# Performance work log

Measured on AMD Instinct MI355X. Metric: run time of the kernel, lower is better.

The kernel has to match this reference:

```python
import jax, jax.numpy as jnp
import numpy as np

IMG_H, IMG_W = 432.0, 768.0
B, N = 8, 1_000_000


def setup_inputs() -> dict:
    key = jax.random.key(0)
    k1, k2 = jax.random.split(key)
    scores = jax.random.uniform(k1, (B, N, 1), dtype=jnp.float32)
    # center-format boxes (x, y, w, h) roughly in image coords so masks fire
    scale = jnp.array([IMG_W, IMG_H, 256.0, 256.0], dtype=jnp.float32)
    rps = jax.random.uniform(k2, (B, N, 4), dtype=jnp.float32) * scale
    return {"scores": scores, "rps": rps, "n_train_pre_nms": 12000}


def _anchors_clip(boxes):
    # boxes: [B, N, 4] in (cx, cy, w, h)
    cx, cy, w, h = boxes[..., 0], boxes[..., 1], boxes[..., 2], boxes[..., 3]
    x1 = jnp.clip(cx - w * 0.5, 0.0, IMG_W)
    x2 = jnp.clip(cx + w * 0.5, 0.0, IMG_W)
    y1 = jnp.clip(cy - h * 0.5, 0.0, IMG_H)
    y2 = jnp.clip(cy + h * 0.5, 0.0, IMG_H)
    nw = x2 - x1
    nh = y2 - y1
    nx = x1 + nw * 0.5
    ny = y1 + nh * 0.5
    return jnp.stack([nx, ny, nw, nh], axis=-1)


def reference(scores, rps, n_train_pre_nms):
    rois = _anchors_clip(rps)                                   # [B, N, 4]
    mask = ((rois[..., 2] > 16.0) & (rois[..., 3] > 16.0))
    s = scores * mask.astype(scores.dtype)[..., None]           # [B, N, 1]
    # full descending argsort along anchor dim, keep top n_train_pre_nms
    order = jnp.argsort(-s[..., 0], axis=1)[:, :n_train_pre_nms]  # [B, K]
    rois_sel = jnp.take_along_axis(rois, order[..., None], axis=1)  # [B, K, 4]
    s_sel = jnp.take_along_axis(s, order[..., None], axis=1)        # [B, K, 1]
    return rois_sel, s_sel
```

## Files before the change

kernel.cpp:

```cpp
#include <hip/hip_runtime.h>
#include <stdint.h>

#define BATCH    8
#define NITEMS   1000000
#define NTHR     125000
#define NBLKS    489
#define NC       64
#define NF       4096
#define NF8      8192
#define SBASE    62
#define THRESH   0.96875f
#define MID63    0.984375f
#define BUFCAP   512
#define CANDCAP  65536
#define CANDCAP2 262144
#define CAPC     131072
#define IMG_W    768.0f
#define IMG_H    432.0f

typedef unsigned long long ull;

static __device__ __forceinline__ float clip0(float v, float hi) {
    return fminf(fmaxf(v, 0.0f), hi);
}
static __device__ __forceinline__ int cbin(float s) {
    int g = (int)(s * (float)NC);
    return g > NC - 1 ? NC - 1 : (g < 0 ? 0 : g);
}
static __device__ __forceinline__ int fbin(float s, int g) {
    int f = (int)(s * (float)(NC * NF)) - g * NF;
    return f > NF - 1 ? NF - 1 : (f < 0 ? 0 : f);
}
static __device__ __forceinline__ unsigned mkbits(float4 box, float s) {
    float x1 = clip0(box.x - box.z * 0.5f, IMG_W);
    float x2 = clip0(box.x + box.z * 0.5f, IMG_W);
    float y1 = clip0(box.y - box.w * 0.5f, IMG_H);
    float y2 = clip0(box.y + box.w * 0.5f, IMG_H);
    bool m = ((x2 - x1) > 16.0f) && ((y2 - y1) > 16.0f);
    return __float_as_uint(m ? s : 0.0f);
}
static __device__ __forceinline__ int g8of(float s) {
    int cb = (s >= MID63) ? 63 : 62;
    return (cb - SBASE) * NF + fbin(s, cb);
}

__global__ __launch_bounds__(256)
void k_scores(const float* __restrict__ scores,
              const float4* __restrict__ rps,
              ull* __restrict__ clist,
              unsigned* __restrict__ fhist8g,
              unsigned* __restrict__ rawCnt,
              unsigned* __restrict__ ovf) {
    __shared__ ull buf[BUFCAP];
    __shared__ unsigned blkCnt, gBase;
    const int b = blockIdx.y, tid = threadIdx.x;
    const int t = blockIdx.x * 256 + tid;
    const int lane = tid & 63;
    if (tid == 0) blkCnt = 0u;
    __syncthreads();
    const float4* sp4 = (const float4*)(scores + (size_t)b * NITEMS);
    float4 a0 = make_float4(0, 0, 0, 0), a1 = make_float4(0, 0, 0, 0);
    const bool act = (t < NTHR);
    if (act) { a0 = sp4[2 * t]; a1 = sp4[2 * t + 1]; }
    float sv[8] = {a0.x, a0.y, a0.z, a0.w, a1.x, a1.y, a1.z, a1.w};
    const int i0 = t * 8;
    #pragma unroll
    for (int j = 0; j < 8; ++j) {
        bool q = act && (sv[j] >= THRESH);
        ull m = __ballot(q);
        if (m) {
            unsigned pre = (unsigned)__popcll(m & ((1ULL << lane) - 1ULL));
            int leader = __ffsll((long long)m) - 1;
            unsigned bse = 0;
            if (lane == leader) bse = atomicAdd(&blkCnt, (unsigned)__popcll(m));
            bse = (unsigned)__shfl((int)bse, leader);
            if (q) {
                unsigned s2 = bse + pre;
                if (s2 < BUFCAP)
                    buf[s2] = ((ull)__float_as_uint(sv[j]) << 32) |
                              (unsigned)(~(unsigned)(i0 + j));
            }
        }
    }
    __syncthreads();
    unsigned n = blkCnt;
    if (n > BUFCAP) { if (tid == 0) atomicOr(&ovf[b], 1u); n = BUFCAP; }
    if (tid == 0) gBase = atomicAdd(&rawCnt[b], n);
    __syncthreads();
    const unsigned gb = gBase;
    for (unsigned i = tid; i < n; i += 256) {
        unsigned slot = gb + i;
        if (slot >= CANDCAP) break;
        ull key = buf[i];
        unsigned idx = ~((unsigned)key);
        float4 box = rps[(size_t)b * NITEMS + idx];
        float s = __uint_as_float((unsigned)(key >> 32));
        if (mkbits(box, s)) {
            atomicAdd(&fhist8g[b * NF8 + g8of(s)], 1u);
            clist[(size_t)b * CANDCAP + slot] = key;
        } else {
            clist[(size_t)b * CANDCAP + slot] = 0ull;
        }
    }
}

__global__ __launch_bounds__(1024)
void k_mid(const float* __restrict__ scores,
           const float4* __restrict__ rps,
           const ull* __restrict__ clist,
           ull* __restrict__ clist2,
           const unsigned* __restrict__ rawCnt,
           const unsigned* __restrict__ ovf,
           const unsigned* __restrict__ fhist8g,
           unsigned* __restrict__ fsuf8g,
           unsigned* __restrict__ csuf64g,
           unsigned* __restrict__ chist64g,
           unsigned* __restrict__ fsufFg,
           unsigned* __restrict__ fhistFg,
           unsigned* __restrict__ meta,
           ull* __restrict__ cand,
           int K) {
    const int b = blockIdx.x, tid = threadIdx.x;
    __shared__ unsigned h[NF8];
    __shared__ unsigned sc[1024];
    __shared__ unsigned smallA[NC], smallB[NC];
    __shared__ unsigned s_fb8, s_tot, s_cbb, s_nab, s_n2;

    unsigned cw[8], pin[8], run = 0;
    const unsigned* hb = fhist8g + b * NF8;
    #pragma unroll
    for (int k = 0; k < 8; ++k) {
        cw[k] = hb[NF8 - 1 - (tid * 8 + k)];
        run += cw[k]; pin[k] = run;
    }
    sc[tid] = run; __syncthreads();
    unsigned x = run;
    for (int off = 1; off < 1024; off <<= 1) {
        unsigned tv = (tid >= off) ? sc[tid - off] : 0u;
        __syncthreads();
        x += tv; sc[tid] = x;
        __syncthreads();
    }
    const unsigned exclBase = x - run;
    const unsigned alive = sc[1023];
    if (tid == 0) { s_fb8 = 0u; s_tot = alive; }
    __syncthreads();
    #pragma unroll
    for (int k = 0; k < 8; ++k) {
        int g = NF8 - 1 - (tid * 8 + k);
        unsigned excl = exclBase + pin[k] - cw[k];
        fsuf8g[b * NF8 + g] = excl;
        h[g] = excl;
        if (excl < (unsigned)K && excl + cw[k] >= (unsigned)K) {
            s_fb8 = (unsigned)g; s_tot = excl + cw[k];
        }
    }
    __syncthreads();
    const unsigned rawN0 = rawCnt[b];
    unsigned N = rawN0 > CANDCAP ? CANDCAP : rawN0;
    const bool fast = (alive >= (unsigned)K) && (ovf[b] == 0u) &&
                      (rawN0 <= (unsigned)CANDCAP) && (s_tot <= (unsigned)CAPC);
    if (tid == 0) {
        meta[b * 8 + 4] = fast ? 1u : 0u;
        meta[b * 8 + 2] = s_fb8;
        meta[b * 8 + 3] = s_tot;
    }
    __syncthreads();
    if (fast) {
        const unsigned fb8v = s_fb8;
        const size_t c0 = (size_t)b * CANDCAP;
        for (unsigned i = tid; i < N; i += 1024) {
            ull key = clist[c0 + i];
            if (!key) continue;
            float s = __uint_as_float((unsigned)(key >> 32));
            int g8 = g8of(s);
            if ((unsigned)g8 < fb8v) continue;
            unsigned slot = atomicAdd(&h[g8], 1u);
            if (slot < CAPC) cand[(size_t)b * CAPC + slot] = key;
        }
        return;
    }
    if (tid < NC) smallA[tid] = 0u;
    __syncthreads();
    const size_t base = (size_t)b * NITEMS;
    for (int i = tid; i < NITEMS; i += 1024) {
        unsigned bits = mkbits(rps[base + i], scores[base + i]);
        if (bits) atomicAdd(&smallA[cbin(__uint_as_float(bits))], 1u);
    }
    __syncthreads();
    if (tid == 0) {
        unsigned runc = 0, cbb = 0, nab = 0; bool found = false;
        for (int g = NC - 1; g >= 0; --g) {
            unsigned c = smallA[g];
            csuf64g[b * NC + g] = runc; chist64g[b * NC + g] = c;
            smallB[g] = runc;
            if (!found && runc < (unsigned)K && runc + c >= (unsigned)K) {
                cbb = (unsigned)g; nab = runc; found = true;
            }
            runc += c;
        }
        s_cbb = cbb; s_nab = nab; s_n2 = 0u;
        meta[b * 8 + 0] = cbb; meta[b * 8 + 1] = nab;
    }
    __syncthreads();
    const unsigned cbb = s_cbb, nab = s_nab;
    if (tid < NC) smallA[tid] = smallB[tid];
    for (int k = tid; k < NF; k += 1024) h[k] = 0u;
    __syncthreads();
    for (int i = tid; i < NITEMS; i += 1024) {
        unsigned bits = mkbits(rps[base + i], scores[base + i]);
        if (!bits) continue;
        float s = __uint_as_float(bits);
        int g = cbin(s);
        if ((unsigned)g < cbb) continue;
        ull key = ((ull)bits << 32) | (unsigned)(~(unsigned)i);
        if ((unsigned)g > cbb) {
            unsigned slot = atomicAdd(&smallA[g], 1u);
            if (slot < CAPC) cand[(size_t)b * CAPC + slot] = key;
        } else {
            unsigned s2 = atomicAdd(&s_n2, 1u);
            if (s2 < CANDCAP2) clist2[(size_t)b * CANDCAP2 + s2] = key;
            atomicAdd(&h[fbin(s, (int)cbb)], 1u);
        }
    }
    __syncthreads();
    unsigned n2 = s_n2 > CANDCAP2 ? CANDCAP2 : s_n2;
    unsigned fcw[4], fpin[4], frun = 0;
    #pragma unroll
    for (int k = 0; k < 4; ++k) {
        fcw[k] = h[NF - 1 - (tid * 4 + k)];
        frun += fcw[k]; fpin[k] = frun;
    }
    sc[tid] = frun; __syncthreads();
    unsigned fx = frun;
    for (int off = 1; off < 1024; off <<= 1) {
        unsigned tv = (tid >= off) ? sc[tid - off] : 0u;
        __syncthreads();
        fx += tv; sc[tid] = fx;
        __syncthreads();
    }
    const unsigned fexcl = fx - frun;
    const unsigned ftot = sc[1023];
    if (tid == 0) { s_fb8 = 0u; s_tot = nab + ftot; }
    __syncthreads();
    #pragma unroll
    for (int k = 0; k < 4; ++k) {
        int g = NF - 1 - (tid * 4 + k);
        unsigned excl = fexcl + fpin[k] - fcw[k];
        fsufFg[b * NF + g] = excl; fhistFg[b * NF + g] = fcw[k];
        unsigned t0 = nab + excl;
        if (t0 < (unsigned)K && t0 + fcw[k] >= (unsigned)K) {
            s_fb8 = (unsigned)g; s_tot = t0 + fcw[k];
        }
        h[g] = nab + excl;
    }
    __syncthreads();
    if (tid == 0) { meta[b * 8 + 2] = s_fb8; meta[b * 8 + 3] = s_tot; }
    __syncthreads();
    const unsigned fbv = s_fb8;
    for (unsigned i = tid; i < n2; i += 1024) {
        ull key = clist2[(size_t)b * CANDCAP2 + i];
        unsigned bits = (unsigned)(key >> 32);
        float s = __uint_as_float(bits);
        int f = fbin(s, (int)cbb);
        if ((unsigned)f < fbv) continue;
        unsigned slot = atomicAdd(&h[f], 1u);
        if (slot < CAPC) cand[(size_t)b * CAPC + slot] = key;
    }
}

__global__ __launch_bounds__(256)
void k_rank_out(const ull* __restrict__ cand,
                const unsigned* __restrict__ meta,
                const unsigned* __restrict__ fsuf8g,
                const unsigned* __restrict__ fhist8g,
                const unsigned* __restrict__ csuf64g,
                const unsigned* __restrict__ chist64g,
                const unsigned* __restrict__ fsufFg,
                const unsigned* __restrict__ fhistFg,
                const float4* __restrict__ rps,
                float* __restrict__ out,
                int K) {
    const int b = blockIdx.y;
    unsigned total = meta[b * 8 + 3];
    if (total > CAPC) total = CAPC;
    const unsigned fast = meta[b * 8 + 4];
    for (unsigned p = blockIdx.x * 256 + threadIdx.x; p < total;
         p += gridDim.x * 256) {
        const ull key = cand[(size_t)b * CAPC + p];
        const float s = __uint_as_float((unsigned)(key >> 32));
        unsigned sbase, scnt;
        if (fast) {
            int g8 = g8of(s);
            sbase = fsuf8g[b * NF8 + g8];
            scnt  = fhist8g[b * NF8 + g8];
        } else {
            const unsigned cbb = meta[b * 8 + 0], nab = meta[b * 8 + 1];
            int g = cbin(s);
            if ((unsigned)g > cbb) {
                sbase = csuf64g[b * NC + g];
                scnt  = chist64g[b * NC + g];
            } else {
                int f = fbin(s, (int)g);
                sbase = nab + fsufFg[b * NF + f];
                scnt  = fhistFg[b * NF + f];
            }
        }
        unsigned send = sbase + scnt;
        if (send > total) send = total;
        unsigned rank = sbase;
        for (unsigned j = sbase; j < send; ++j)
            rank += (cand[(size_t)b * CAPC + j] > key) ? 1u : 0u;
        if (rank < (unsigned)K) {
            unsigned idx = ~((unsigned)key);
            if (idx >= (unsigned)NITEMS) idx = 0;
            float4 box = rps[(size_t)b * NITEMS + idx];
            float x1 = clip0(box.x - box.z * 0.5f, IMG_W);
            float x2 = clip0(box.x + box.z * 0.5f, IMG_W);
            float y1 = clip0(box.y - box.w * 0.5f, IMG_H);
            float y2 = clip0(box.y + box.w * 0.5f, IMG_H);
            float nw = x2 - x1, nh = y2 - y1;
            float nx = x1 + nw * 0.5f, ny = y1 + nh * 0.5f;
            ((float4*)out)[(size_t)b * K + rank] = make_float4(nx, ny, nw, nh);
            out[(size_t)BATCH * K * 4 + (size_t)b * K + rank] = s;
        }
    }
}

extern "C" void kernel_launch(void* const* d_in, const int* in_sizes, int n_in,
                              void* d_out, int out_size, void* d_ws, size_t ws_size,
                              hipStream_t stream) {
    const float*  scores = (const float*)d_in[0];
    const float4* rps    = (const float4*)d_in[1];
    const int K = out_size / (BATCH * 5);

    uint8_t* w = (uint8_t*)d_ws;
    ull* clist        = (ull*)(w);
    ull* cand         = (ull*)(w +  4500000);
    ull* clist2       = (ull*)(w + 13000000);
    unsigned* fhist8g = (unsigned*)(w + 30000000);
    unsigned* rawCnt  = (unsigned*)(w + 30262144);
    unsigned* ovf     = (unsigned*)(w + 30262176);
    unsigned* fsuf8g  = (unsigned*)(w + 30400000);
    unsigned* meta    = (unsigned*)(w + 30700000);
    unsigned* csuf64g = (unsigned*)(w + 30701000);
    unsigned* chist64g= (unsigned*)(w + 30704000);
    unsigned* fsufFg  = (unsigned*)(w + 30710000);
    unsigned* fhistFg = (unsigned*)(w + 30850000);

    hipMemsetAsync(fhist8g, 0, 262208, stream);
    k_scores<<<dim3(NBLKS, BATCH), dim3(256), 0, stream>>>(scores, rps, clist,
                                                           fhist8g, rawCnt, ovf);
    k_mid<<<dim3(BATCH), dim3(1024), 0, stream>>>(scores, rps, clist, clist2,
                                                  rawCnt, ovf, fhist8g, fsuf8g,
                                                  csuf64g, chist64g, fsufFg, fhistFg,
                                                  meta, cand, K);
    k_rank_out<<<dim3(128, BATCH), dim3(256), 0, stream>>>(cand, meta, fsuf8g, fhist8g,
                                                           csuf64g, chist64g, fsufFg,
                                                           fhistFg, rps,
                                                           (float*)d_out, K);
}
```

Baseline: 91.74 us.

## Build fine histogram in k_mid shared memory instead of global atomics

Moves the fine-bin histogram construction from global atomics in k_scores into a shared-memory histogram pass inside k_mid, which rereads the candidate list. The 256KB memset is replaced by a tiny zeroing kernel that only clears the counters, and k_mid writes the histogram out for later kernels. This removes global atomic contention and a large memset, at the cost of an extra candidate-list scan in the single-block-per-batch k_mid.

```diff
diff --git a/kernel.cpp b/kernel.cpp
--- a/kernel.cpp
+++ b/kernel.cpp
@@ -44,11 +44,15 @@
     return (cb - SBASE) * NF + fbin(s, cb);
 }
 
+__global__ __launch_bounds__(64)
+void k_zero(unsigned* __restrict__ rawCnt, unsigned* __restrict__ ovf) {
+    if (threadIdx.x < BATCH) { rawCnt[threadIdx.x] = 0u; ovf[threadIdx.x] = 0u; }
+}
+
 __global__ __launch_bounds__(256)
 void k_scores(const float* __restrict__ scores,
               const float4* __restrict__ rps,
               ull* __restrict__ clist,
-              unsigned* __restrict__ fhist8g,
               unsigned* __restrict__ rawCnt,
               unsigned* __restrict__ ovf) {
     __shared__ ull buf[BUFCAP];
@@ -95,12 +99,7 @@
         unsigned idx = ~((unsigned)key);
         float4 box = rps[(size_t)b * NITEMS + idx];
         float s = __uint_as_float((unsigned)(key >> 32));
-        if (mkbits(box, s)) {
-            atomicAdd(&fhist8g[b * NF8 + g8of(s)], 1u);
-            clist[(size_t)b * CANDCAP + slot] = key;
-        } else {
-            clist[(size_t)b * CANDCAP + slot] = 0ull;
-        }
+        clist[(size_t)b * CANDCAP + slot] = mkbits(box, s) ? key : 0ull;
     }
 }
 
@@ -111,7 +110,7 @@
            ull* __restrict__ clist2,
            const unsigned* __restrict__ rawCnt,
            const unsigned* __restrict__ ovf,
-           const unsigned* __restrict__ fhist8g,
+           unsigned* __restrict__ fhist8g,
            unsigned* __restrict__ fsuf8g,
            unsigned* __restrict__ csuf64g,
            unsigned* __restrict__ chist64g,
@@ -126,11 +125,22 @@
     __shared__ unsigned smallA[NC], smallB[NC];
     __shared__ unsigned s_fb8, s_tot, s_cbb, s_nab, s_n2;
 
+    for (int k = tid; k < NF8; k += 1024) h[k] = 0u;
+    __syncthreads();
+    const unsigned rawN0 = rawCnt[b];
+    unsigned N = rawN0 > CANDCAP ? CANDCAP : rawN0;
+    const size_t c0 = (size_t)b * CANDCAP;
+    for (unsigned i = tid; i < N; i += 1024) {
+        ull key = clist[c0 + i];
+        if (!key) continue;
+        float s = __uint_as_float((unsigned)(key >> 32));
+        atomicAdd(&h[g8of(s)], 1u);
+    }
+    __syncthreads();
     unsigned cw[8], pin[8], run = 0;
-    const unsigned* hb = fhist8g + b * NF8;
     #pragma unroll
     for (int k = 0; k < 8; ++k) {
-        cw[k] = hb[NF8 - 1 - (tid * 8 + k)];
+        cw[k] = h[NF8 - 1 - (tid * 8 + k)];
         run += cw[k]; pin[k] = run;
     }
     sc[tid] = run; __syncthreads();
@@ -150,14 +160,18 @@
         int g = NF8 - 1 - (tid * 8 + k);
         unsigned excl = exclBase + pin[k] - cw[k];
         fsuf8g[b * NF8 + g] = excl;
-        h[g] = excl;
+        fhist8g[b * NF8 + g] = cw[k];
         if (excl < (unsigned)K && excl + cw[k] >= (unsigned)K) {
             s_fb8 = (unsigned)g; s_tot = excl + cw[k];
         }
     }
     __syncthreads();
-    const unsigned rawN0 = rawCnt[b];
-    unsigned N = rawN0 > CANDCAP ? CANDCAP : rawN0;
+    #pragma unroll
+    for (int k = 0; k < 8; ++k) {
+        int g = NF8 - 1 - (tid * 8 + k);
+        h[g] = exclBase + pin[k] - cw[k];
+    }
+    __syncthreads();
     const bool fast = (alive >= (unsigned)K) && (ovf[b] == 0u) &&
                       (rawN0 <= (unsigned)CANDCAP) && (s_tot <= (unsigned)CAPC);
     if (tid == 0) {
@@ -168,7 +182,6 @@
     __syncthreads();
     if (fast) {
         const unsigned fb8v = s_fb8;
-        const size_t c0 = (size_t)b * CANDCAP;
         for (unsigned i = tid; i < N; i += 1024) {
             ull key = clist[c0 + i];
             if (!key) continue;
@@ -348,9 +361,9 @@
     unsigned* fsufFg  = (unsigned*)(w + 30710000);
     unsigned* fhistFg = (unsigned*)(w + 30850000);
 
-    hipMemsetAsync(fhist8g, 0, 262208, stream);
+    k_zero<<<dim3(1), dim3(64), 0, stream>>>(rawCnt, ovf);
     k_scores<<<dim3(NBLKS, BATCH), dim3(256), 0, stream>>>(scores, rps, clist,
-                                                           fhist8g, rawCnt, ovf);
+                                                           rawCnt, ovf);
     k_mid<<<dim3(BATCH), dim3(1024), 0, stream>>>(scores, rps, clist, clist2,
                                                   rawCnt, ovf, fhist8g, fsuf8g,
                                                   csuf64g, chist64g, fsufFg, fhistFg,
```

Measured after the change: 98.32 us. 7.2% more time.

## Fuse mid and rank kernels, drop global atomics and memset via per-block slots

Applied to the files above, without the earlier changes.

Each score block now writes its candidates into a fixed per-block slot region and records its count, instead of reserving global space with atomics and building a global histogram with atomics. The 8-block mid kernel rebuilds the fine histogram in shared memory, scatters candidates, and then ranks and writes the outputs itself, so the separate rank kernel and the memset are gone. Launch overhead and global atomic traffic go down, but the ranking phase now runs on only 8 blocks instead of 1024. The per-block buffer shrinks to 128 entries and the candidate capacity to 32768, which pushes more inputs onto the slow fallback path if those limits are exceeded.

```diff
diff --git a/kernel.cpp b/kernel.cpp
--- a/kernel.cpp
+++ b/kernel.cpp
@@ -5,16 +5,15 @@
 #define NITEMS   1000000
 #define NTHR     125000
 #define NBLKS    489
+#define BUFCAP   128
 #define NC       64
 #define NF       4096
 #define NF8      8192
 #define SBASE    62
 #define THRESH   0.96875f
 #define MID63    0.984375f
-#define BUFCAP   512
-#define CANDCAP  65536
+#define CAPC     32768
 #define CANDCAP2 262144
-#define CAPC     131072
 #define IMG_W    768.0f
 #define IMG_H    432.0f
 
@@ -48,17 +47,15 @@
 void k_scores(const float* __restrict__ scores,
               const float4* __restrict__ rps,
               ull* __restrict__ clist,
-              unsigned* __restrict__ fhist8g,
-              unsigned* __restrict__ rawCnt,
-              unsigned* __restrict__ ovf) {
+              unsigned* __restrict__ blkCnt) {
     __shared__ ull buf[BUFCAP];
-    __shared__ unsigned blkCnt, gBase;
-    const int b = blockIdx.y, tid = threadIdx.x;
-    const int t = blockIdx.x * 256 + tid;
+    __shared__ unsigned cnt;
+    const int b = blockIdx.y, blk = blockIdx.x, tid = threadIdx.x;
     const int lane = tid & 63;
-    if (tid == 0) blkCnt = 0u;
+    if (tid == 0) cnt = 0u;
     __syncthreads();
     const float4* sp4 = (const float4*)(scores + (size_t)b * NITEMS);
+    const int t = blk * 256 + tid;
     float4 a0 = make_float4(0, 0, 0, 0), a1 = make_float4(0, 0, 0, 0);
     const bool act = (t < NTHR);
     if (act) { a0 = sp4[2 * t]; a1 = sp4[2 * t + 1]; }
@@ -72,7 +69,7 @@
             unsigned pre = (unsigned)__popcll(m & ((1ULL << lane) - 1ULL));
             int leader = __ffsll((long long)m) - 1;
             unsigned bse = 0;
-            if (lane == leader) bse = atomicAdd(&blkCnt, (unsigned)__popcll(m));
+            if (lane == leader) bse = atomicAdd(&cnt, (unsigned)__popcll(m));
             bse = (unsigned)__shfl((int)bse, leader);
             if (q) {
                 unsigned s2 = bse + pre;
@@ -83,54 +80,57 @@
         }
     }
     __syncthreads();
-    unsigned n = blkCnt;
-    if (n > BUFCAP) { if (tid == 0) atomicOr(&ovf[b], 1u); n = BUFCAP; }
-    if (tid == 0) gBase = atomicAdd(&rawCnt[b], n);
-    __syncthreads();
-    const unsigned gb = gBase;
+    unsigned n = cnt;
+    if (tid == 0) blkCnt[b * NBLKS + blk] = n;
+    if (n > BUFCAP) n = BUFCAP;
+    const size_t base = ((size_t)b * NBLKS + blk) * BUFCAP;
     for (unsigned i = tid; i < n; i += 256) {
-        unsigned slot = gb + i;
-        if (slot >= CANDCAP) break;
         ull key = buf[i];
         unsigned idx = ~((unsigned)key);
         float4 box = rps[(size_t)b * NITEMS + idx];
         float s = __uint_as_float((unsigned)(key >> 32));
-        if (mkbits(box, s)) {
-            atomicAdd(&fhist8g[b * NF8 + g8of(s)], 1u);
-            clist[(size_t)b * CANDCAP + slot] = key;
-        } else {
-            clist[(size_t)b * CANDCAP + slot] = 0ull;
-        }
+        clist[base + i] = mkbits(box, s) ? key : 0ull;
     }
 }
 
 __global__ __launch_bounds__(1024)
-void k_mid(const float* __restrict__ scores,
-           const float4* __restrict__ rps,
-           const ull* __restrict__ clist,
-           ull* __restrict__ clist2,
-           const unsigned* __restrict__ rawCnt,
-           const unsigned* __restrict__ ovf,
-           const unsigned* __restrict__ fhist8g,
-           unsigned* __restrict__ fsuf8g,
-           unsigned* __restrict__ csuf64g,
-           unsigned* __restrict__ chist64g,
-           unsigned* __restrict__ fsufFg,
-           unsigned* __restrict__ fhistFg,
-           unsigned* __restrict__ meta,
-           ull* __restrict__ cand,
-           int K) {
+void k_mega(const float* __restrict__ scores,
+            const float4* __restrict__ rps,
+            const ull* __restrict__ clist,
+            const unsigned* __restrict__ blkCnt,
+            ull* __restrict__ cand,
+            ull* __restrict__ clist2,
+            float* __restrict__ out,
+            int K) {
     const int b = blockIdx.x, tid = threadIdx.x;
-    __shared__ unsigned h[NF8];
+    __shared__ unsigned hsuf[NF8];
+    __shared__ unsigned hctr[NF8];
     __shared__ unsigned sc[1024];
-    __shared__ unsigned smallA[NC], smallB[NC];
-    __shared__ unsigned s_fb8, s_tot, s_cbb, s_nab, s_n2;
-
+    __shared__ unsigned bc[576];
+    __shared__ unsigned s_fb8, s_tot, s_ovf, s_cbb, s_nab, s_n2;
+
+    for (int k = tid; k < NBLKS; k += 1024) bc[k] = blkCnt[b * NBLKS + k];
+    for (int k = tid; k < NF8; k += 1024) hctr[k] = 0u;
+    if (tid == 0) s_ovf = 0u;
+    __syncthreads();
+    unsigned myovf = 0u;
+    for (int k = tid; k < NBLKS; k += 1024) if (bc[k] > BUFCAP) myovf = 1u;
+    if (myovf) atomicOr(&s_ovf, 1u);
+    const size_t c0 = (size_t)b * NBLKS * BUFCAP;
+    for (unsigned u = tid; u < NBLKS * BUFCAP; u += 1024) {
+        unsigned kb = u / BUFCAP, i = u - kb * BUFCAP;
+        unsigned n = bc[kb]; if (n > BUFCAP) n = BUFCAP;
+        if (i >= n) continue;
+        ull key = clist[c0 + u];
+        if (!key) continue;
+        float s = __uint_as_float((unsigned)(key >> 32));
+        atomicAdd(&hctr[g8of(s)], 1u);
+    }
+    __syncthreads();
     unsigned cw[8], pin[8], run = 0;
-    const unsigned* hb = fhist8g + b * NF8;
     #pragma unroll
     for (int k = 0; k < 8; ++k) {
-        cw[k] = hb[NF8 - 1 - (tid * 8 + k)];
+        cw[k] = hctr[NF8 - 1 - (tid * 8 + k)];
         run += cw[k]; pin[k] = run;
     }
     sc[tid] = run; __syncthreads();
@@ -149,63 +149,81 @@
     for (int k = 0; k < 8; ++k) {
         int g = NF8 - 1 - (tid * 8 + k);
         unsigned excl = exclBase + pin[k] - cw[k];
-        fsuf8g[b * NF8 + g] = excl;
-        h[g] = excl;
+        hsuf[g] = excl;
+        hctr[g] = excl;
         if (excl < (unsigned)K && excl + cw[k] >= (unsigned)K) {
             s_fb8 = (unsigned)g; s_tot = excl + cw[k];
         }
     }
     __syncthreads();
-    const unsigned rawN0 = rawCnt[b];
-    unsigned N = rawN0 > CANDCAP ? CANDCAP : rawN0;
-    const bool fast = (alive >= (unsigned)K) && (ovf[b] == 0u) &&
-                      (rawN0 <= (unsigned)CANDCAP) && (s_tot <= (unsigned)CAPC);
-    if (tid == 0) {
-        meta[b * 8 + 4] = fast ? 1u : 0u;
-        meta[b * 8 + 2] = s_fb8;
-        meta[b * 8 + 3] = s_tot;
-    }
-    __syncthreads();
+    const bool fast = (alive >= (unsigned)K) && (s_ovf == 0u) &&
+                      (s_tot <= (unsigned)CAPC);
     if (fast) {
         const unsigned fb8v = s_fb8;
-        const size_t c0 = (size_t)b * CANDCAP;
-        for (unsigned i = tid; i < N; i += 1024) {
-            ull key = clist[c0 + i];
+        for (unsigned u = tid; u < NBLKS * BUFCAP; u += 1024) {
+            unsigned kb = u / BUFCAP, i = u - kb * BUFCAP;
+            unsigned n = bc[kb]; if (n > BUFCAP) n = BUFCAP;
+            if (i >= n) continue;
+            ull key = clist[c0 + u];
             if (!key) continue;
             float s = __uint_as_float((unsigned)(key >> 32));
             int g8 = g8of(s);
             if ((unsigned)g8 < fb8v) continue;
-            unsigned slot = atomicAdd(&h[g8], 1u);
+            unsigned slot = atomicAdd(&hctr[g8], 1u);
             if (slot < CAPC) cand[(size_t)b * CAPC + slot] = key;
         }
+        __syncthreads();
+        unsigned total = s_tot;
+        for (unsigned p = tid; p < total; p += 1024) {
+            ull key = cand[(size_t)b * CAPC + p];
+            float s = __uint_as_float((unsigned)(key >> 32));
+            int g8 = g8of(s);
+            unsigned sbase = hsuf[g8];
+            unsigned send = hctr[g8];
+            if (send > total) send = total;
+            unsigned rank = sbase;
+            for (unsigned j = sbase; j < send; ++j)
+                rank += (cand[(size_t)b * CAPC + j] > key) ? 1u : 0u;
+            if (rank < (unsigned)K) {
+                unsigned idx = ~((unsigned)key);
+                if (idx >= (unsigned)NITEMS) idx = 0;
+                float4 box = rps[(size_t)b * NITEMS + idx];
+                float x1 = clip0(box.x - box.z * 0.5f, IMG_W);
+                float x2 = clip0(box.x + box.z * 0.5f, IMG_W);
+                float y1 = clip0(box.y - box.w * 0.5f, IMG_H);
+                float y2 = clip0(box.y + box.w * 0.5f, IMG_H);
+                float nw = x2 - x1, nh = y2 - y1;
+                ((float4*)out)[(size_t)b * K + rank] =
+                    make_float4(x1 + nw * 0.5f, y1 + nh * 0.5f, nw, nh);
+                out[(size_t)BATCH * K * 4 + (size_t)b * K + rank] = s;
+            }
+        }
         return;
     }
-    if (tid < NC) smallA[tid] = 0u;
+    if (tid < NC) bc[tid] = 0u;
     __syncthreads();
     const size_t base = (size_t)b * NITEMS;
     for (int i = tid; i < NITEMS; i += 1024) {
         unsigned bits = mkbits(rps[base + i], scores[base + i]);
-        if (bits) atomicAdd(&smallA[cbin(__uint_as_float(bits))], 1u);
+        if (bits) atomicAdd(&bc[cbin(__uint_as_float(bits))], 1u);
     }
     __syncthreads();
     if (tid == 0) {
-        unsigned runc = 0, cbb = 0, nab = 0; bool found = false;
+        unsigned runc = 0, cbbv = 0, nabv = 0; bool found = false;
         for (int g = NC - 1; g >= 0; --g) {
-            unsigned c = smallA[g];
-            csuf64g[b * NC + g] = runc; chist64g[b * NC + g] = c;
-            smallB[g] = runc;
+            unsigned c = bc[g];
+            bc[64 + g] = runc;
             if (!found && runc < (unsigned)K && runc + c >= (unsigned)K) {
-                cbb = (unsigned)g; nab = runc; found = true;
+                cbbv = (unsigned)g; nabv = runc; found = true;
             }
             runc += c;
         }
-        s_cbb = cbb; s_nab = nab; s_n2 = 0u;
-        meta[b * 8 + 0] = cbb; meta[b * 8 + 1] = nab;
+        s_cbb = cbbv; s_nab = nabv; s_n2 = 0u;
     }
     __syncthreads();
     const unsigned cbb = s_cbb, nab = s_nab;
-    if (tid < NC) smallA[tid] = smallB[tid];
-    for (int k = tid; k < NF; k += 1024) h[k] = 0u;
+    if (tid < NC) hsuf[NF + tid] = bc[64 + tid];
+    for (int k = tid; k < NF; k += 1024) hctr[k] = 0u;
     __syncthreads();
     for (int i = tid; i < NITEMS; i += 1024) {
         unsigned bits = mkbits(rps[base + i], scores[base + i]);
@@ -215,12 +233,12 @@
         if ((unsigned)g < cbb) continue;
         ull key = ((ull)bits << 32) | (unsigned)(~(unsigned)i);
         if ((unsigned)g > cbb) {
-            unsigned slot = atomicAdd(&smallA[g], 1u);
+            unsigned slot = atomicAdd(&bc[64 + g], 1u);
             if (slot < CAPC) cand[(size_t)b * CAPC + slot] = key;
         } else {
             unsigned s2 = atomicAdd(&s_n2, 1u);
             if (s2 < CANDCAP2) clist2[(size_t)b * CANDCAP2 + s2] = key;
-            atomicAdd(&h[fbin(s, (int)cbb)], 1u);
+            atomicAdd(&hctr[fbin(s, (int)cbb)], 1u);
         }
     }
     __syncthreads();
@@ -228,7 +246,7 @@
     unsigned fcw[4], fpin[4], frun = 0;
     #pragma unroll
     for (int k = 0; k < 4; ++k) {
-        fcw[k] = h[NF - 1 - (tid * 4 + k)];
+        fcw[k] = hctr[NF - 1 - (tid * 4 + k)];
         frun += fcw[k]; fpin[k] = frun;
     }
     sc[tid] = frun; __syncthreads();
@@ -247,66 +265,37 @@
     for (int k = 0; k < 4; ++k) {
         int g = NF - 1 - (tid * 4 + k);
         unsigned excl = fexcl + fpin[k] - fcw[k];
-        fsufFg[b * NF + g] = excl; fhistFg[b * NF + g] = fcw[k];
+        hsuf[g] = nab + excl;
         unsigned t0 = nab + excl;
         if (t0 < (unsigned)K && t0 + fcw[k] >= (unsigned)K) {
             s_fb8 = (unsigned)g; s_tot = t0 + fcw[k];
         }
-        h[g] = nab + excl;
-    }
-    __syncthreads();
-    if (tid == 0) { meta[b * 8 + 2] = s_fb8; meta[b * 8 + 3] = s_tot; }
+    }
+    __syncthreads();
+    #pragma unroll
+    for (int k = 0; k < 4; ++k) {
+        int g = NF - 1 - (tid * 4 + k);
+        hctr[g] = hsuf[g];
+    }
     __syncthreads();
     const unsigned fbv = s_fb8;
     for (unsigned i = tid; i < n2; i += 1024) {
         ull key = clist2[(size_t)b * CANDCAP2 + i];
-        unsigned bits = (unsigned)(key >> 32);
-        float s = __uint_as_float(bits);
+        float s = __uint_as_float((unsigned)(key >> 32));
         int f = fbin(s, (int)cbb);
         if ((unsigned)f < fbv) continue;
-        unsigned slot = atomicAdd(&h[f], 1u);
+        unsigned slot = atomicAdd(&hctr[f], 1u);
         if (slot < CAPC) cand[(size_t)b * CAPC + slot] = key;
     }
-}
-
-__global__ __launch_bounds__(256)
-void k_rank_out(const ull* __restrict__ cand,
-                const unsigned* __restrict__ meta,
-                const unsigned* __restrict__ fsuf8g,
-                const unsigned* __restrict__ fhist8g,
-                const unsigned* __restrict__ csuf64g,
-                const unsigned* __restrict__ chist64g,
-                const unsigned* __restrict__ fsufFg,
-                const unsigned* __restrict__ fhistFg,
-                const float4* __restrict__ rps,
-                float* __restrict__ out,
-                int K) {
-    const int b = blockIdx.y;
-    unsigned total = meta[b * 8 + 3];
-    if (total > CAPC) total = CAPC;
-    const unsigned fast = meta[b * 8 + 4];
-    for (unsigned p = blockIdx.x * 256 + threadIdx.x; p < total;
-         p += gridDim.x * 256) {
-        const ull key = cand[(size_t)b * CAPC + p];
-        const float s = __uint_as_float((unsigned)(key >> 32));
-        unsigned sbase, scnt;
-        if (fast) {
-            int g8 = g8of(s);
-            sbase = fsuf8g[b * NF8 + g8];
-            scnt  = fhist8g[b * NF8 + g8];
-        } else {
-            const unsigned cbb = meta[b * 8 + 0], nab = meta[b * 8 + 1];
-            int g = cbin(s);
-            if ((unsigned)g > cbb) {
-                sbase = csuf64g[b * NC + g];
-                scnt  = chist64g[b * NC + g];
-            } else {
-                int f = fbin(s, (int)g);
-                sbase = nab + fsufFg[b * NF + f];
-                scnt  = fhistFg[b * NF + f];
-            }
-        }
-        unsigned send = sbase + scnt;
+    __syncthreads();
+    unsigned total = s_tot > CAPC ? CAPC : s_tot;
+    for (unsigned p = tid; p < total; p += 1024) {
+        ull key = cand[(size_t)b * CAPC + p];
+        float s = __uint_as_float((unsigned)(key >> 32));
+        int g = cbin(s);
+        unsigned sbase, send;
+        if ((unsigned)g > cbb) { sbase = hsuf[NF + g]; send = bc[64 + g]; }
+        else { int f = fbin(s, (int)g); sbase = hsuf[f]; send = hctr[f]; }
         if (send > total) send = total;
         unsigned rank = sbase;
         for (unsigned j = sbase; j < send; ++j)
@@ -320,8 +309,8 @@
             float y1 = clip0(box.y - box.w * 0.5f, IMG_H);
             float y2 = clip0(box.y + box.w * 0.5f, IMG_H);
             float nw = x2 - x1, nh = y2 - y1;
-            float nx = x1 + nw * 0.5f, ny = y1 + nh * 0.5f;
-            ((float4*)out)[(size_t)b * K + rank] = make_float4(nx, ny, nw, nh);
+            ((float4*)out)[(size_t)b * K + rank] =
+                make_float4(x1 + nw * 0.5f, y1 + nh * 0.5f, nw, nh);
             out[(size_t)BATCH * K * 4 + (size_t)b * K + rank] = s;
         }
     }
@@ -335,28 +324,12 @@
     const int K = out_size / (BATCH * 5);
 
     uint8_t* w = (uint8_t*)d_ws;
-    ull* clist        = (ull*)(w);
-    ull* cand         = (ull*)(w +  4500000);
-    ull* clist2       = (ull*)(w + 13000000);
-    unsigned* fhist8g = (unsigned*)(w + 30000000);
-    unsigned* rawCnt  = (unsigned*)(w + 30262144);
-    unsigned* ovf     = (unsigned*)(w + 30262176);
-    unsigned* fsuf8g  = (unsigned*)(w + 30400000);
-    unsigned* meta    = (unsigned*)(w + 30700000);
-    unsigned* csuf64g = (unsigned*)(w + 30701000);
-    unsigned* chist64g= (unsigned*)(w + 30704000);
-    unsigned* fsufFg  = (unsigned*)(w + 30710000);
-    unsigned* fhistFg = (unsigned*)(w + 30850000);
-
-    hipMemsetAsync(fhist8g, 0, 262208, stream);
-    k_scores<<<dim3(NBLKS, BATCH), dim3(256), 0, stream>>>(scores, rps, clist,
-                                                           fhist8g, rawCnt, ovf);
-    k_mid<<<dim3(BATCH), dim3(1024), 0, stream>>>(scores, rps, clist, clist2,
-                                                  rawCnt, ovf, fhist8g, fsuf8g,
-                                                  csuf64g, chist64g, fsufFg, fhistFg,
-                                                  meta, cand, K);
-    k_rank_out<<<dim3(128, BATCH), dim3(256), 0, stream>>>(cand, meta, fsuf8g, fhist8g,
-                                                           csuf64g, chist64g, fsufFg,
-                                                           fhistFg, rps,
-                                                           (float*)d_out, K);
-}
+    ull* clist       = (ull*)(w);
+    unsigned* blkCnt = (unsigned*)(w + 4100000);
+    ull* cand        = (ull*)(w + 4200000);
+    ull* clist2      = (ull*)(w + 6400000);
+
+    k_scores<<<dim3(NBLKS, BATCH), dim3(256), 0, stream>>>(scores, rps, clist, blkCnt);
+    k_mega<<<dim3(BATCH), dim3(1024), 0, stream>>>(scores, rps, clist, blkCnt,
+                                                   cand, clist2, (float*)d_out, K);
+}
```

Result: slower. 100.6 us (+9.7%).
